# Optimization experiments

Hardware: AMD Instinct MI355X
Metric: run time of the kernel (lower is better)

The kernel has to match this reference:

```python
import jax, jax.numpy as jnp
import numpy as np
from jax import lax

EPS = 1e-5
PATCH = 4

def _ln(x, g, b):
    m = jnp.mean(x, -1, keepdims=True)
    v = jnp.mean(jnp.square(x - m), -1, keepdims=True)
    return (x - m) * lax.rsqrt(v + EPS) * g + b

def _gelu(x):
    return jax.nn.gelu(x, approximate=False)  # torch nn.GELU default (erf)

def setup_inputs() -> dict:
    key = jax.random.key(0)
    B, D, H, M, L, C = 8, 256, 16, 1024, 24, 1000
    S = (32 // PATCH) ** 2 + 1  # 65 tokens
    ks = iter(jax.random.split(key, 16))
    def w(shape, fan_in):
        return jax.random.normal(next(ks), shape, jnp.float32) * (fan_in ** -0.5)
    z = lambda *s: jnp.zeros(s, jnp.float32)
    o = lambda *s: jnp.ones(s, jnp.float32)
    return {
        'x': jax.random.normal(next(ks), (B, 3, 32, 32), jnp.float32),
        'conv_w': w((D, 3, PATCH, PATCH), 3 * PATCH * PATCH),
        'conv_b': z(D),
        'cls_tok': jax.random.normal(next(ks), (1, 1, D), jnp.float32),
        'pos_emb': jax.random.normal(next(ks), (1, S, D), jnp.float32),
        'Wqkv': w((L, H, D, 3 * D), D),   # per-layer, per-head full-D qkv
        'bqkv': z(L, H, 3 * D),
        'Wo': w((L, H * D, D), H * D),
        'bo': z(L, D),
        'ln1_g': o(L, D), 'ln1_b': z(L, D),
        'ln2_g': o(L, D), 'ln2_b': z(L, D),
        'Wm1': w((L, D, M), D), 'bm1': z(L, M),
        'Wm2': w((L, M, D), M), 'bm2': z(L, D),
        'Wh1': w((D, M), D), 'bh1': z(M),
        'Wh2': w((M, D), M), 'bh2': z(D),
        'Wh3': w((D, C), D), 'bh3': z(C),
    }

def reference(x, conv_w, conv_b, cls_tok, pos_emb, Wqkv, bqkv, Wo, bo,
              ln1_g, ln1_b, ln2_g, ln2_b, Wm1, bm1, Wm2, bm2,
              Wh1, bh1, Wh2, bh2, Wh3, bh3):
    B = x.shape[0]
    D = conv_w.shape[0]
    H = Wqkv.shape[1]
    scale = (D / H) ** -0.5  # quirk: full-D attention scaled by head_dim
    # patch embed: conv stride=kernel=PATCH, then flatten HW -> tokens
    y = lax.conv_general_dilated(x, conv_w, (PATCH, PATCH), 'VALID',
                                 dimension_numbers=('NCHW', 'OIHW', 'NCHW'))
    y = y + conv_b[None, :, None, None]
    y = y.reshape(B, D, -1).transpose(0, 2, 1)  # [B, N, D]
    y = jnp.concatenate([jnp.broadcast_to(cls_tok, (B, 1, D)), y], axis=1) + pos_emb
    S = y.shape[1]

    def layer(carry, p):
        Wq, bq, Wo_, bo_, g1, b1_, g2, b2_, W1, bm1_, W2, bm2_ = p
        z = _ln(carry, g1, b1_)
        qkv = jnp.einsum('bsd,hde->bhse', z, Wq) + bq[None, :, None, :]  # [B,H,S,3D]
        q, k, v = jnp.split(qkv, 3, axis=-1)
        attn = jax.nn.softmax(jnp.einsum('bhsd,bhtd->bhst', q, k) * scale, axis=-1)
        o = jnp.einsum('bhst,bhtd->bhsd', attn, v)
        o = o.transpose(0, 2, 1, 3).reshape(B, S, -1)  # concat heads -> [B,S,H*D]
        y1 = o @ Wo_ + bo_ + carry
        z2 = _ln(y1, g2, b2_)
        h = _gelu(_gelu(z2 @ W1 + bm1_) @ W2 + bm2_)  # GELU after BOTH linears
        return h + y1, None

    y, _ = lax.scan(layer, y, (Wqkv, bqkv, Wo, bo, ln1_g, ln1_b, ln2_g, ln2_b,
                               Wm1, bm1, Wm2, bm2))
    cls = y[:, 0, :]
    h = _gelu(cls @ Wh1 + bh1)
    h = _gelu(h @ Wh2 + bh2)
    return h @ Wh3 + bh3
```

## Files before the change

kernel.cpp:

```cpp
#include <hip/hip_runtime.h>
#include <hip/hip_bf16.h>

typedef __attribute__((ext_vector_type(8))) short short8;
typedef __attribute__((ext_vector_type(4))) float f32x4;

__device__ __forceinline__ float gelu_f(float x) {
  return 0.5f * x * (1.0f + erff(x * 0.70710678118654752440f));
}
__device__ __forceinline__ short f2bf(float f) {
  unsigned u = __float_as_uint(f);
  u += 0x7fffu + ((u >> 16) & 1u);
  return (short)(u >> 16);
}
__device__ __forceinline__ float bf2f(short s) {
  return __uint_as_float(((unsigned)(unsigned short)s) << 16);
}
__device__ __forceinline__ void split2(float v, short& h, short& l) {
  h = f2bf(v);
  l = f2bf(v - bf2f(h));
}
__device__ __forceinline__ int swz(int col, int row) {
  return (col & ~63) | ((col & 63) ^ ((row & 7) << 3));
}

__device__ __forceinline__ float block_sum_256(float v, float* sb) {
#pragma unroll
  for (int o = 1; o < 64; o <<= 1) v += __shfl_xor(v, o, 64);
  if ((threadIdx.x & 63) == 0) sb[threadIdx.x >> 6] = v;
  __syncthreads();
  float r = sb[0] + sb[1] + sb[2] + sb[3];
  __syncthreads();
  return r;
}

struct PrepArgs {
  const float *x, *cw, *cb, *cls, *pos, *ln1g, *ln1b;
  float* tok;
  short *zh, *zl;
  const float *Wqkv, *Wo, *Wm1, *Wm2;
  short *Wqh, *Wql, *Woh, *Wol, *W1h, *W1l, *W2h, *W2l;
};

__device__ void conv_body(const float* __restrict__ in,
                          short* __restrict__ outh, short* __restrict__ outl,
                          int K, int ldn, int group, long long gstride, int bx,
                          int by, float* tile ) {
  const int n0 = bx * 128;
  const int k0 = by * 64;
  const int tid = threadIdx.x;
  {
    const int j = tid & 31;
    const int kb = tid >> 5;
    const int n = n0 + 4 * j;
    const long long nbase = (long long)(n / group) * gstride + (n % group);
#pragma unroll
    for (int i = 0; i < 8; ++i) {
      const int k = kb * 8 + i;
      float4 v4 = *(const float4*)(in + nbase + (long long)(k0 + k) * ldn);
      tile[0 * 2112 + k * 33 + j] = v4.x;
      tile[1 * 2112 + k * 33 + j] = v4.y;
      tile[2 * 2112 + k * 33 + j] = v4.z;
      tile[3 * 2112 + k * 33 + j] = v4.w;
    }
  }
  __syncthreads();
  {
    const int r = tid >> 1;
    const int hf = tid & 1;
    const int n = n0 + r;
    const int e = r & 3, jj = r >> 2;
    const int g8 = n & 7;
    const float* te = tile + e * 2112 + jj;
    const long long obase = (long long)n * K + k0;
#pragma unroll
    for (int j2 = 0; j2 < 4; ++j2) {
      const int s = hf * 4 + j2;
      const int m = s ^ g8;
      short8 sh, sl;
#pragma unroll
      for (int e8 = 0; e8 < 8; ++e8) {
        float v = te[(m * 8 + e8) * 33];
        short h, L;
        split2(v, h, L);
        sh[e8] = h;
        sl[e8] = L;
      }
      *(short8*)(outh + obase + s * 8) = sh;
      *(short8*)(outl + obase + s * 8) = sl;
    }
  }
  __syncthreads();
}

__global__ __launch_bounds__(256) void prep_kernel(PrepArgs p) {
  __shared__ __align__(16) float smem[4 * 64 * 33];
  const int t = blockIdx.x;
  if (t < 520) {
    float* sb = smem;
    int r = t;
    int b = r / 65, s = r % 65;
    int d = threadIdx.x;
    float val;
    if (s == 0) {
      val = p.cls[d];
    } else {
      int pp = s - 1, pi = pp >> 3, pj = pp & 7;
      const float* xb = p.x + b * 3072 + pi * 4 * 32 + pj * 4;
      const float* w = p.cw + d * 48;
      float acc = p.cb[d];
#pragma unroll
      for (int c = 0; c < 3; ++c)
#pragma unroll
        for (int i = 0; i < 4; ++i)
#pragma unroll
          for (int j = 0; j < 4; ++j)
            acc += xb[c * 1024 + i * 32 + j] * w[c * 16 + i * 4 + j];
      val = acc;
    }
    val += p.pos[s * 256 + d];
    p.tok[r * 256 + d] = val;
    float mean = block_sum_256(val, sb) * (1.0f / 256.0f);
    float dv = val - mean;
    float var = block_sum_256(dv * dv, sb) * (1.0f / 256.0f);
    float z = dv * rsqrtf(var + 1e-5f) * p.ln1g[d] + p.ln1b[d];
    short h, L;
    split2(z, h, L);
    p.zh[r * 256 + swz(d, r)] = h;
    p.zl[r * 256 + swz(d, r)] = L;
    return;
  }
  const int u = t - 520;
  const int layer = u / 576;
  const int r = u % 576;
  if (r < 384) {
    conv_body(p.Wqkv + (long long)layer * 3145728,
              p.Wqh + (long long)layer * 3145728,
              p.Wql + (long long)layer * 3145728, 256, 768, 768, 196608LL,
              r % 96, r / 96, smem);
  } else if (r < 512) {
    int v = r - 384;
    conv_body(p.Wo + (long long)layer * 1048576,
              p.Woh + (long long)layer * 1048576,
              p.Wol + (long long)layer * 1048576, 4096, 256, 1 << 30, 0LL,
              v % 2, v / 2, smem);
  } else if (r < 544) {
    int v = r - 512;
    conv_body(p.Wm1 + (long long)layer * 262144,
              p.W1h + (long long)layer * 262144,
              p.W1l + (long long)layer * 262144, 256, 1024, 1 << 30, 0LL,
              v % 8, v / 8, smem);
  } else {
    int v = r - 544;
    conv_body(p.Wm2 + (long long)layer * 262144,
              p.W2h + (long long)layer * 262144,
              p.W2l + (long long)layer * 262144, 1024, 256, 1 << 30, 0LL,
              v % 2, v / 2, smem);
  }
}

__global__ __launch_bounds__(256) void gemm_x3(
    const short* __restrict__ Ah, const short* __restrict__ Al,
    const short* __restrict__ Bh, const short* __restrict__ Bl, int M, int N,
    int K, int kchunk, const float* __restrict__ bias,
    float* __restrict__ out32, float* __restrict__ P) {
  __shared__ short Ash[128 * 64];
  __shared__ short Asl[128 * 64];
  __shared__ short Bsh[128 * 64];
  __shared__ short Bsl[128 * 64];
  const int tid = threadIdx.x;
  const int w = tid >> 6, l = tid & 63;
  const int col0 = blockIdx.x * 128;
  const int row0 = blockIdx.y * 128;
  const int kbeg = blockIdx.z * kchunk;
  const int kend = kbeg + kchunk;
  const int wm = w >> 1, wn = w & 1;

  f32x4 acc[4][4];
#pragma unroll
  for (int i = 0; i < 4; ++i)
#pragma unroll
    for (int j = 0; j < 4; ++j) acc[i][j] = (f32x4)(0.f);

  const int srow = l >> 3;
  const int sslot = l & 7;

#define STAGE4(dst, src, rbase)                                            \
  {                                                                        \
    _Pragma("unroll") for (int i = 0; i < 4; ++i) {                        \
      int r = (w * 4 + i) * 8 + srow;                                      \
      const char* gp =                                                     \
          (const char*)(src + (size_t)(rbase + r) * K + k0) + sslot * 16;  \
      short* lp = dst + (w * 4 + i) * 512;                                 \
      __builtin_amdgcn_global_load_lds(                                    \
          (const __attribute__((address_space(1))) unsigned int*)gp,       \
          (__attribute__((address_space(3))) unsigned int*)lp, 16, 0, 0);  \
    }                                                                      \
  }

  for (int k0 = kbeg; k0 < kend; k0 += 64) {
    __syncthreads();
    STAGE4(Ash, Ah, row0)
    STAGE4(Asl, Al, row0)
    STAGE4(Bsh, Bh, col0)
    STAGE4(Bsl, Bl, col0)
    __syncthreads();
#pragma unroll
    for (int kc = 0; kc < 2; ++kc) {
      short8 ah[4], al[4], bh[4], bl[4];
#pragma unroll
      for (int mi = 0; mi < 4; ++mi) {
        int row = wm * 64 + mi * 16 + (l & 15);
        int slot = (kc * 4 + (l >> 4)) ^ (row & 7);
        ah[mi] = *(const short8*)&Ash[row * 64 + slot * 8];
        al[mi] = *(const short8*)&Asl[row * 64 + slot * 8];
      }
#pragma unroll
      for (int ni = 0; ni < 4; ++ni) {
        int row = wn * 64 + ni * 16 + (l & 15);
        int slot = (kc * 4 + (l >> 4)) ^ (row & 7);
        bh[ni] = *(const short8*)&Bsh[row * 64 + slot * 8];
        bl[ni] = *(const short8*)&Bsl[row * 64 + slot * 8];
      }
#pragma unroll
      for (int mi = 0; mi < 4; ++mi)
#pragma unroll
        for (int ni = 0; ni < 4; ++ni) {
          acc[mi][ni] = __builtin_amdgcn_mfma_f32_16x16x32_bf16(
              ah[mi], bh[ni], acc[mi][ni], 0, 0, 0);
          acc[mi][ni] = __builtin_amdgcn_mfma_f32_16x16x32_bf16(
              ah[mi], bl[ni], acc[mi][ni], 0, 0, 0);
          acc[mi][ni] = __builtin_amdgcn_mfma_f32_16x16x32_bf16(
              al[mi], bh[ni], acc[mi][ni], 0, 0, 0);
        }
    }
  }
#undef STAGE4

#pragma unroll
  for (int mi = 0; mi < 4; ++mi) {
#pragma unroll
    for (int ni = 0; ni < 4; ++ni) {
      int row = row0 + wm * 64 + mi * 16 + (l >> 4) * 4;
      int col = col0 + wn * 64 + ni * 16 + (l & 15);
      if (out32) {
        float bc = bias ? bias[col] : 0.f;
#pragma unroll
        for (int r = 0; r < 4; ++r)
          if (row + r < M)
            out32[(size_t)(row + r) * N + col] = acc[mi][ni][r] + bc;
      } else {
        float* Pz = P + (size_t)blockIdx.z * M * N;
#pragma unroll
        for (int r = 0; r < 4; ++r)
          if (row + r < M) Pz[(size_t)(row + r) * N + col] = acc[mi][ni][r];
      }
    }
  }
}

template <int NSPLIT>
__global__ __launch_bounds__(256) void epilogue_kernel(
    const float* __restrict__ P, int M, int N, const float* __restrict__ bias,
    const float* __restrict__ res, float* __restrict__ out32,
    short* __restrict__ o16h, short* __restrict__ o16l, int act,
    const float* __restrict__ g, const float* __restrict__ bln,
    short* __restrict__ z16h, short* __restrict__ z16l) {
  __shared__ float sb[4];
  int r = blockIdx.x;
  float myval = 0.f;
  for (int c = threadIdx.x; c < N; c += 256) {
    const float* pp = P + (long long)r * N + c;
    float acc = 0.f;
#pragma unroll
    for (int s = 0; s < NSPLIT; ++s) acc += pp[(long long)s * M * N];
    acc += bias[c];
    if (act) acc = gelu_f(acc);
    if (res) acc += res[(long long)r * N + c];
    if (out32) out32[(long long)r * N + c] = acc;
    if (o16h) {
      short h, L;
      split2(acc, h, L);
      o16h[(long long)r * N + swz(c, r)] = h;
      o16l[(long long)r * N + swz(c, r)] = L;
    }
    myval = acc;
  }
  if (z16h) {
    float mean = block_sum_256(myval, sb) * (1.f / 256.f);
    float dv = myval - mean;
    float var = block_sum_256(dv * dv, sb) * (1.f / 256.f);
    float z = dv * rsqrtf(var + 1e-5f) * g[threadIdx.x] + bln[threadIdx.x];
    short h, L;
    split2(z, h, L);
    z16h[r * 256 + swz((int)threadIdx.x, r)] = h;
    z16l[r * 256 + swz((int)threadIdx.x, r)] = L;
  }
}

#define AROWS 17
__global__ __launch_bounds__(256) void attn_kernel(const float* __restrict__ qkv,
                                                   short* __restrict__ Oh,
                                                   short* __restrict__ Ol) {
  __shared__ float qs[AROWS + 1][256];
  __shared__ float Ks[68][68];
  __shared__ float ps[AROWS][66];
  const int tid = threadIdx.x;
  const int s0 = blockIdx.x * AROWS;
  const int bh = blockIdx.y;
  const int b = bh >> 4, h = bh & 15;
  const long long base = (long long)(b * 65) * 12288 + h * 768;

#pragma unroll
  for (int i = 0; i < AROWS; ++i) {
    int s = s0 + i;
    qs[i][tid] = (s < 65) ? qkv[base + (long long)s * 12288 + tid] : 0.f;
  }

  const int up = tid / 17, tg = tid % 17;
  const int i0 = up * 2, t0 = tg * 4;
  const bool uval = (tid < 153);
  float acc[2][4] = {};
  for (int dc = 0; dc < 256; dc += 64) {
    __syncthreads();
    for (int idx = tid; idx < 65 * 64; idx += 256) {
      int t = idx >> 6, dd = idx & 63;
      Ks[t][dd] = qkv[base + (long long)t * 12288 + 256 + dc + dd];
    }
    __syncthreads();
    if (uval) {
#pragma unroll
      for (int d4 = 0; d4 < 64; d4 += 4) {
        float4 qa = *(const float4*)&qs[i0][dc + d4];
        float4 qb = *(const float4*)&qs[i0 + 1][dc + d4];
#pragma unroll
        for (int c = 0; c < 4; ++c) {
          float4 kv = *(const float4*)&Ks[t0 + c][d4];
          acc[0][c] += qa.x * kv.x + qa.y * kv.y + qa.z * kv.z + qa.w * kv.w;
          acc[1][c] += qb.x * kv.x + qb.y * kv.y + qb.z * kv.z + qb.w * kv.w;
        }
      }
    }
  }
  if (uval) {
#pragma unroll
    for (int ii = 0; ii < 2; ++ii) {
      int i = i0 + ii;
      if (i < AROWS && (s0 + i) < 65) {
#pragma unroll
        for (int c = 0; c < 4; ++c) {
          int t = t0 + c;
          if (t < 65) ps[i][t] = acc[ii][c] * 0.25f;
        }
      }
    }
  }
  __syncthreads();

  if (tid < AROWS && (s0 + tid) < 65) {
    float* row = ps[tid];
    float m = row[0];
    for (int t = 1; t < 65; ++t) m = fmaxf(m, row[t]);
    float sum = 0.f;
    for (int t = 0; t < 65; ++t) {
      float e = expf(row[t] - m);
      row[t] = e;
      sum += e;
    }
    float inv = 1.f / sum;
    for (int t = 0; t < 65; ++t) row[t] *= inv;
  }
  __syncthreads();

  float oacc[AROWS];
#pragma unroll
  for (int i = 0; i < AROWS; ++i) oacc[i] = 0.f;
  const float* vp = qkv + base + 512 + tid;
  for (int t = 0; t < 65; ++t) {
    float vtd = vp[(long long)t * 12288];
#pragma unroll
    for (int i = 0; i < AROWS; ++i) oacc[i] += ps[i][t] * vtd;
  }
#pragma unroll
  for (int i = 0; i < AROWS; ++i) {
    int s = s0 + i;
    if (s < 65) {
      int row = b * 65 + s;
      int col = h * 256 + ((tid & ~63) | ((tid & 63) ^ ((row & 7) << 3)));
      short hh, LL;
      split2(oacc[i], hh, LL);
      Oh[(long long)row * 4096 + col] = hh;
      Ol[(long long)row * 4096 + col] = LL;
    }
  }
}

template <int KS>
__global__ __launch_bounds__(256) void head_gemm2(
    const float* __restrict__ A, int lda, const float* __restrict__ B,
    const float* __restrict__ bias, float* __restrict__ C, int N, int K,
    int act) {
  constexpr int COLS = 256 / KS;
  __shared__ float red[KS][COLS];
  const int lane = threadIdx.x % COLS;
  const int ks = threadIdx.x / COLS;
  const int c = blockIdx.x * COLS + lane;
  const int r = blockIdx.y;
  const float* a = A + (long long)r * lda;
  float acc = 0.f;
  const int kc = K / KS;
  if (c < N) {
    const float* ap = a + ks * kc;
    const float* bp = B + (long long)(ks * kc) * N + c;
#pragma unroll 8
    for (int k = 0; k < kc; ++k) acc += ap[k] * bp[(long long)k * N];
  }
  red[ks][lane] = acc;
  __syncthreads();
  if (ks == 0 && c < N) {
    float v = bias[c];
#pragma unroll
    for (int s = 0; s < KS; ++s) v += red[s][lane];
    if (act) v = gelu_f(v);
    C[(long long)r * N + c] = v;
  }
}

extern "C" void kernel_launch(void* const* d_in, const int* in_sizes, int n_in,
                              void* d_out, int out_size, void* d_ws,
                              size_t ws_size, hipStream_t stream) {
  const float* x = (const float*)d_in[0];
  const float* conv_w = (const float*)d_in[1];
  const float* conv_b = (const float*)d_in[2];
  const float* cls = (const float*)d_in[3];
  const float* pos = (const float*)d_in[4];
  const float* Wqkv = (const float*)d_in[5];
  const float* bqkv = (const float*)d_in[6];
  const float* Wo = (const float*)d_in[7];
  const float* bo = (const float*)d_in[8];
  const float* ln1g = (const float*)d_in[9];
  const float* ln1b = (const float*)d_in[10];
  const float* ln2g = (const float*)d_in[11];
  const float* ln2b = (const float*)d_in[12];
  const float* Wm1 = (const float*)d_in[13];
  const float* bm1 = (const float*)d_in[14];
  const float* Wm2 = (const float*)d_in[15];
  const float* bm2 = (const float*)d_in[16];
  const float* Wh1 = (const float*)d_in[17];
  const float* bh1 = (const float*)d_in[18];
  const float* Wh2 = (const float*)d_in[19];
  const float* bh2 = (const float*)d_in[20];
  const float* Wh3 = (const float*)d_in[21];
  const float* bh3 = (const float*)d_in[22];
  float* out = (float*)d_out;

  float* ws = (float*)d_ws;
  float* tok = ws;
  float* y1 = ws + 163840;
  float* Pb = ws + 327680;
  float* qkvf = ws + 2457600;
  short* zh = (short*)(ws + 8847360);
  short* zl = (short*)(ws + 8929280);
  short* Oh = (short*)(ws + 9011200);
  short* Ol = (short*)(ws + 10321920);
  short* h1h = (short*)(ws + 11632640);
  short* h1l = (short*)(ws + 11960320);
  float* hh1 = ws + 12288000;
  float* hh2 = ws + 12296192;
  short* Wqh = (short*)(ws + 12298240);
  short* Wql = (short*)(ws + 50046976);
  short* Woh = (short*)(ws + 87795712);
  short* Wol_ = (short*)(ws + 100378624);
  short* W1h = (short*)(ws + 112961536);
  short* W1l = (short*)(ws + 116107264);
  short* W2h = (short*)(ws + 119252992);
  short* W2l = (short*)(ws + 122398720);

  const int M = 520;

  PrepArgs p;
  p.x = x; p.cw = conv_w; p.cb = conv_b; p.cls = cls; p.pos = pos;
  p.ln1g = ln1g; p.ln1b = ln1b;
  p.tok = tok; p.zh = zh; p.zl = zl;
  p.Wqkv = Wqkv; p.Wo = Wo; p.Wm1 = Wm1; p.Wm2 = Wm2;
  p.Wqh = Wqh; p.Wql = Wql; p.Woh = Woh; p.Wol = Wol_;
  p.W1h = W1h; p.W1l = W1l; p.W2h = W2h; p.W2l = W2l;
  prep_kernel<<<520 + 24 * 576, 256, 0, stream>>>(p);

  for (int l = 0; l < 24; ++l) {
    const short* Wqhl = Wqh + (long long)l * 3145728;
    const short* Wqll = Wql + (long long)l * 3145728;
    const short* Wohl = Woh + (long long)l * 1048576;
    const short* Woll = Wol_ + (long long)l * 1048576;
    const short* W1hl = W1h + (long long)l * 262144;
    const short* W1ll = W1l + (long long)l * 262144;
    const short* W2hl = W2h + (long long)l * 262144;
    const short* W2ll = W2l + (long long)l * 262144;
    const float* bq = bqkv + l * 12288;
    const float* bol = bo + l * 256;
    const float* b1 = bm1 + l * 1024;
    const float* b2 = bm2 + l * 256;

    gemm_x3<<<dim3(96, 5, 1), 256, 0, stream>>>(zh, zl, Wqhl, Wqll, M, 12288,
                                                256, 256, bq, qkvf, nullptr);

    attn_kernel<<<dim3(4, 128), 256, 0, stream>>>(qkvf, Oh, Ol);

    gemm_x3<<<dim3(2, 5, 16), 256, 0, stream>>>(Oh, Ol, Wohl, Woll, M, 256,
                                                4096, 256, nullptr, nullptr,
                                                Pb);
    epilogue_kernel<16><<<520, 256, 0, stream>>>(
        Pb, M, 256, bol, tok, y1, nullptr, nullptr, 0, ln2g + l * 256,
        ln2b + l * 256, zh, zl);

    gemm_x3<<<dim3(8, 5, 4), 256, 0, stream>>>(zh, zl, W1hl, W1ll, M, 1024,
                                               256, 64, nullptr, nullptr, Pb);
    epilogue_kernel<4><<<520, 256, 0, stream>>>(Pb, M, 1024, b1, nullptr,
                                                nullptr, h1h, h1l, 1, nullptr,
                                                nullptr, nullptr, nullptr);

    gemm_x3<<<dim3(2, 5, 16), 256, 0, stream>>>(h1h, h1l, W2hl, W2ll, M, 256,
                                                1024, 64, nullptr, nullptr,
                                                Pb);
    const float* ng = (l < 23) ? ln1g + (l + 1) * 256 : nullptr;
    const float* nb = (l < 23) ? ln1b + (l + 1) * 256 : nullptr;
    short* nzh = (l < 23) ? zh : nullptr;
    short* nzl = (l < 23) ? zl : nullptr;
    epilogue_kernel<16><<<520, 256, 0, stream>>>(Pb, M, 256, b2, y1, tok,
                                                 nullptr, nullptr, 1, ng, nb,
                                                 nzh, nzl);
  }

  head_gemm2<4><<<dim3(16, 8), 256, 0, stream>>>(tok, 16640, Wh1, bh1, hh1,
                                                 1024, 256, 1);
  head_gemm2<8><<<dim3(8, 8), 256, 0, stream>>>(hh1, 1024, Wh2, bh2, hh2, 256,
                                                1024, 1);
  head_gemm2<4><<<dim3(16, 8), 256, 0, stream>>>(hh2, 256, Wh3, bh3, out, 1000,
                                                 256, 0);
}
```

Baseline: 3.091 ms.

## Fuse MLP1 bias+GELU+bf16 split into GEMM epilogue, drop split-K

The first MLP GEMM now runs without split-K and writes bias+GELU output directly as swizzled hi/lo bf16 pairs from its epilogue, removing the partial-sum buffer round trip and a separate epilogue launch per layer. The prep kernel's transpose tile gets a padded stride and loses a trailing barrier. This trades fewer launches and less global traffic for fewer blocks (40 instead of 160) on that GEMM and scattered 2-byte stores.

```diff
diff --git a/kernel.cpp b/kernel.cpp
--- a/kernel.cpp
+++ b/kernel.cpp
@@ -57,10 +57,10 @@
     for (int i = 0; i < 8; ++i) {
       const int k = kb * 8 + i;
       float4 v4 = *(const float4*)(in + nbase + (long long)(k0 + k) * ldn);
-      tile[0 * 2112 + k * 33 + j] = v4.x;
-      tile[1 * 2112 + k * 33 + j] = v4.y;
-      tile[2 * 2112 + k * 33 + j] = v4.z;
-      tile[3 * 2112 + k * 33 + j] = v4.w;
+      tile[0 * 2113 + k * 33 + j] = v4.x;
+      tile[1 * 2113 + k * 33 + j] = v4.y;
+      tile[2 * 2113 + k * 33 + j] = v4.z;
+      tile[3 * 2113 + k * 33 + j] = v4.w;
     }
   }
   __syncthreads();
@@ -70,7 +70,7 @@
     const int n = n0 + r;
     const int e = r & 3, jj = r >> 2;
     const int g8 = n & 7;
-    const float* te = tile + e * 2112 + jj;
+    const float* te = tile + e * 2113 + jj;
     const long long obase = (long long)n * K + k0;
 #pragma unroll
     for (int j2 = 0; j2 < 4; ++j2) {
@@ -89,11 +89,10 @@
       *(short8*)(outl + obase + s * 8) = sl;
     }
   }
-  __syncthreads();
 }
 
 __global__ __launch_bounds__(256) void prep_kernel(PrepArgs p) {
-  __shared__ __align__(16) float smem[4 * 64 * 33];
+  __shared__ __align__(16) float smem[4 * 2113];
   const int t = blockIdx.x;
   if (t < 520) {
     float* sb = smem;
@@ -162,7 +161,8 @@
     const short* __restrict__ Ah, const short* __restrict__ Al,
     const short* __restrict__ Bh, const short* __restrict__ Bl, int M, int N,
     int K, int kchunk, const float* __restrict__ bias,
-    float* __restrict__ out32, float* __restrict__ P) {
+    float* __restrict__ out32, short* __restrict__ o16h,
+    short* __restrict__ o16l, int act, float* __restrict__ P) {
   __shared__ short Ash[128 * 64];
   __shared__ short Asl[128 * 64];
   __shared__ short Bsh[128 * 64];
@@ -248,6 +248,18 @@
         for (int r = 0; r < 4; ++r)
           if (row + r < M)
             out32[(size_t)(row + r) * N + col] = acc[mi][ni][r] + bc;
+      } else if (o16h) {
+        float bc = bias ? bias[col] : 0.f;
+#pragma unroll
+        for (int r = 0; r < 4; ++r)
+          if (row + r < M) {
+            float v = acc[mi][ni][r] + bc;
+            if (act) v = gelu_f(v);
+            short h, L;
+            split2(v, h, L);
+            o16h[(size_t)(row + r) * N + swz(col, row + r)] = h;
+            o16l[(size_t)(row + r) * N + swz(col, row + r)] = L;
+          }
       } else {
         float* Pz = P + (size_t)blockIdx.z * M * N;
 #pragma unroll
@@ -500,27 +512,26 @@
     const float* b1 = bm1 + l * 1024;
     const float* b2 = bm2 + l * 256;
 
-    gemm_x3<<<dim3(96, 5, 1), 256, 0, stream>>>(zh, zl, Wqhl, Wqll, M, 12288,
-                                                256, 256, bq, qkvf, nullptr);
+    gemm_x3<<<dim3(96, 5, 1), 256, 0, stream>>>(
+        zh, zl, Wqhl, Wqll, M, 12288, 256, 256, bq, qkvf, nullptr, nullptr, 0,
+        nullptr);
 
     attn_kernel<<<dim3(4, 128), 256, 0, stream>>>(qkvf, Oh, Ol);
 
-    gemm_x3<<<dim3(2, 5, 16), 256, 0, stream>>>(Oh, Ol, Wohl, Woll, M, 256,
-                                                4096, 256, nullptr, nullptr,
-                                                Pb);
+    gemm_x3<<<dim3(2, 5, 16), 256, 0, stream>>>(
+        Oh, Ol, Wohl, Woll, M, 256, 4096, 256, nullptr, nullptr, nullptr,
+        nullptr, 0, Pb);
     epilogue_kernel<16><<<520, 256, 0, stream>>>(
         Pb, M, 256, bol, tok, y1, nullptr, nullptr, 0, ln2g + l * 256,
         ln2b + l * 256, zh, zl);
 
-    gemm_x3<<<dim3(8, 5, 4), 256, 0, stream>>>(zh, zl, W1hl, W1ll, M, 1024,
-                                               256, 64, nullptr, nullptr, Pb);
-    epilogue_kernel<4><<<520, 256, 0, stream>>>(Pb, M, 1024, b1, nullptr,
-                                                nullptr, h1h, h1l, 1, nullptr,
-                                                nullptr, nullptr, nullptr);
-
-    gemm_x3<<<dim3(2, 5, 16), 256, 0, stream>>>(h1h, h1l, W2hl, W2ll, M, 256,
-                                                1024, 64, nullptr, nullptr,
-                                                Pb);
+    gemm_x3<<<dim3(8, 5, 1), 256, 0, stream>>>(
+        zh, zl, W1hl, W1ll, M, 1024, 256, 256, b1, nullptr, h1h, h1l, 1,
+        nullptr);
+
+    gemm_x3<<<dim3(2, 5, 16), 256, 0, stream>>>(
+        h1h, h1l, W2hl, W2ll, M, 256, 1024, 64, nullptr, nullptr, nullptr,
+        nullptr, 0, Pb);
     const float* ng = (l < 23) ? ln1g + (l + 1) * 256 : nullptr;
     const float* nb = (l < 23) ? ln1b + (l + 1) * 256 : nullptr;
     short* nzh = (l < 23) ? zh : nullptr;
```

Result: slower. 3.805 ms (+23.1%).
